# Kernel optimization log

Measured on AMD Instinct MI355X. Metric: run time of the kernel, lower is better.

## Reference

```python
import jax, jax.numpy as jnp
import numpy as np

WIDTH = 384
STEP_SIZE = 0.1  # hard-coded in EnergyBlock.__init__
EPS = 1e-5


def conv1d(x, w):
    # x: [B, Cin, L], w: [Cout, Cin, K], stride 1, SAME padding (padding=1 for k=3)
    return jax.lax.conv_general_dilated(
        x, w, window_strides=(1,), padding='SAME',
        dimension_numbers=('NCH', 'OIH', 'NCH'))


def layer_norm_cl(x):
    # torch layer_norm over shape[1:] == normalize jointly over (C, L) per batch elem,
    # no affine params, biased variance.
    mu = jnp.mean(x, axis=(1, 2), keepdims=True)
    var = jnp.mean(jnp.square(x - mu), axis=(1, 2), keepdims=True)
    return (x - mu) * jax.lax.rsqrt(var + EPS)


def energy_block(cat, op_w):
    # cat: [B, width+1, L] = concat(interim_thought, x)
    xl = layer_norm_cl(cat[:, :WIDTH])          # post-LN x (the grad variable)
    c = conv1d(cat, op_w)                        # operator(inputs): no path through xl
    # Ex = sum(c * xl) + sum(where(xl>=0, xl^2, 0))
    # dEx/dxl = c + 2*relu(xl)  (analytic; matches torch.autograd.grad)
    grads = c + 2.0 * jnp.maximum(xl, 0.0)
    return xl - STEP_SIZE * grads


def _init_conv(key, cout, cin, k=3):
    scale = (1.0 / (cin * k)) ** 0.5
    return jax.random.uniform(key, (cout, cin, k), jnp.float32, -scale, scale)


def setup_inputs() -> dict:
    key = jax.random.key(0)
    ks = jax.random.split(key, 6)
    B, L = 32, 512
    return {
        'x': jax.random.normal(ks[0], (B, 1, L), jnp.float32),
        'iters_to_do': 16,
        'proj_w': _init_conv(ks[1], WIDTH, 1),
        'op_w': _init_conv(ks[2], WIDTH, WIDTH + 1),
        'h1_w': _init_conv(ks[3], WIDTH, WIDTH),
        'h2_w': _init_conv(ks[4], WIDTH // 2, WIDTH),
        'h3_w': _init_conv(ks[5], 2, WIDTH // 2),
    }


def reference(x, iters_to_do, proj_w, op_w, h1_w, h2_w, h3_w):
    relu = jax.nn.relu
    interim = relu(conv1d(x, proj_w))  # initial_thought [B, width, L]

    def step(it, _):
        cat = jnp.concatenate([it, x], axis=1)       # recall=True
        new_it = energy_block(cat, op_w)
        out = conv1d(relu(conv1d(relu(conv1d(new_it, h1_w)), h2_w)), h3_w)  # [B,2,L]
        return new_it, out

    _, outs = jax.lax.scan(step, interim, None, length=iters_to_do)
    # eval mode: return all_outputs [B, iters, 2, L]
    return jnp.transpose(outs, (1, 0, 2, 3))
```

## Files before the change

kernel.cpp:

```cpp
#include <hip/hip_runtime.h>
#include <hip/hip_bf16.h>

#define BB 32
#define WW 384
#define LL 512
#define ITERS 16
#define NPB (WW * LL)
#define LROWS 514
#define RP (LROWS * 8)

typedef __attribute__((ext_vector_type(8))) short bf16x8;
typedef __attribute__((ext_vector_type(4))) float f32x4;

__device__ __forceinline__ float b2f(short s) {
    unsigned u = ((unsigned)(unsigned short)s) << 16;
    float f;
    __builtin_memcpy(&f, &u, 4);
    return f;
}
__device__ __forceinline__ short f2b(float v) {
    __hip_bfloat16 h = __float2bfloat16(v);
    return *(short*)&h;
}

__device__ __forceinline__ void gld16(const short* g, short* l) {
    __builtin_amdgcn_global_load_lds(
        (const __attribute__((address_space(1))) unsigned int*)g,
        (__attribute__((address_space(3))) unsigned int*)l, 16, 0, 0);
}

__global__ void wsplit_op(const float* __restrict__ w, short* __restrict__ wh) {
    int i = blockIdx.x * 256 + threadIdx.x;
    if (i >= 3 * 48 * 384 * 8) return;
    int e = i & 7, co = (i >> 3) % 384, oct = (i >> 3) / 384 % 48,
        tap = i / (8 * 384 * 48);
    int ci = oct * 8 + e;
    wh[i] = f2b(w[(co * 385 + ci) * 3 + tap]);
}

__global__ void wx_prep(const float* __restrict__ w, float* __restrict__ wx) {
    int i = blockIdx.x * 256 + threadIdx.x;
    if (i >= 3 * 384) return;
    int co = i % 384, tap = i / 384;
    wx[tap * 384 + co] = w[(co * 385 + 384) * 3 + tap];
}

__global__ void wsplit_h(const float* __restrict__ w, short* __restrict__ wh,
                         int COD, int CO_real) {
    int i = blockIdx.x * 256 + threadIdx.x;
    if (i >= 3 * 48 * COD * 8) return;
    int e = i & 7, co = (i >> 3) % COD, oct = (i >> 3) / COD % 48,
        tap = i / (8 * COD * 48);
    int ci = oct * 8 + e;
    float v = (co < CO_real) ? w[(co * 384 + ci) * 3 + tap] : 0.f;
    wh[i] = f2b(v);
}

__global__ void init_rows(short* itAh, short* itAl, short* itBh, short* itBl,
                          short* a1A, short* a1B, short* a2A, short* a2B) {
    int row = (blockIdx.x & 1) ? (LROWS - 1) : 0;
    int b = blockIdx.x >> 1;
    int tid = threadIdx.x;
    for (int i = tid; i < 48 * 8; i += 64) {
        size_t o = (size_t)b * 48 * RP + (size_t)(i >> 3) * RP + row * 8 + (i & 7);
        itAh[o] = 0; itAl[o] = 0; itBh[o] = 0; itBl[o] = 0;
        a1A[o] = 0; a1B[o] = 0;
    }
    for (int i = tid; i < 24 * 8; i += 64) {
        size_t o = (size_t)b * 24 * RP + (size_t)(i >> 3) * RP + row * 8 + (i & 7);
        a2A[o] = 0; a2B[o] = 0;
    }
}

__global__ void zero_part(float* part, int n) {
    int i = blockIdx.x * 256 + threadIdx.x;
    if (i < n) part[i] = 0.f;
}

__global__ __launch_bounds__(256) void proj_relu(const float* __restrict__ x,
                                                 const float* __restrict__ wp,
                                                 short* __restrict__ oh,
                                                 short* __restrict__ ol,
                                                 float* __restrict__ part) {
    int b = blockIdx.x >> 3, sl = blockIdx.x & 7;
    int tid = threadIdx.x;
    __shared__ float ws[WW * 3];
    __shared__ float xs[66];
    for (int i = tid; i < WW * 3; i += 256) ws[i] = wp[i];
    int l0 = sl * 64;
    for (int i = tid; i < 66; i += 256) {
        int l = l0 + i - 1;
        xs[i] = (l >= 0 && l < LL) ? x[b * LL + l] : 0.f;
    }
    __syncthreads();
    size_t sb = (size_t)b * 48 * RP;
    float s = 0.f, sq = 0.f;
    for (int idx = tid; idx < 64 * WW; idx += 256) {
        int lo = idx / WW, co = idx % WW;
        float v = fmaxf(ws[co * 3] * xs[lo] + ws[co * 3 + 1] * xs[lo + 1] +
                            ws[co * 3 + 2] * xs[lo + 2], 0.f);
        size_t o = sb + (size_t)(co >> 3) * RP + (l0 + lo + 1) * 8 + (co & 7);
        __hip_bfloat16 h = __float2bfloat16(v);
        oh[o] = *(short*)&h;
        ol[o] = f2b(v - __bfloat162float(h));
        s += v; sq += v * v;
    }
    #pragma unroll
    for (int off = 32; off > 0; off >>= 1) {
        s += __shfl_down(s, off);
        sq += __shfl_down(sq, off);
    }
    __shared__ float sr[8];
    int w = tid >> 6;
    if ((tid & 63) == 0) { sr[w] = s; sr[4 + w] = sq; }
    __syncthreads();
    if (tid == 0) {
        atomicAdd(&part[b * 2], sr[0] + sr[1] + sr[2] + sr[3]);
        atomicAdd(&part[b * 2 + 1], sr[4] + sr[5] + sr[6] + sr[7]);
    }
}


#define MMAC(A, B, MT, NT)                                                 \
    acc[MT][NT] = __builtin_amdgcn_mfma_f32_16x16x32_bf16(A, B,            \
                                                          acc[MT][NT], 0, 0, 0);

#define STAGE(KC, TB)                                                      \
    do {                                                                   \
        short* sb_ = smem + (TB) * ASZ;                                    \
        _Pragma("unroll")                                                  \
        for (int r_ = 0; r_ < (ANS + 3) / 4; r_++) {                       \
            int s_ = r_ * 4 + wn;                                          \
            if (s_ < ANS) {                                                \
                int u0_ = s_ * 64;                                         \
                if (u0_ > AU - 64) u0_ = AU - 64;                          \
                int u_ = u0_ + lane;                                       \
                int oc_ = u_ / TLROWS;                                     \
                int rw_ = u_ - oc_ * TLROWS;                               \
                gld16(inh + ibase + (size_t)((KC) * 4 + oc_) * RP +        \
                          (size_t)(l0 + rw_) * 8,                          \
                      sb_ + u0_ * 8);                                      \
            }                                                              \
        }                                                                  \
    } while (0)

#define DECL_B(S) bf16x8 fb0##S, fb1##S, fb2##S, fb3##S;

#define LOADB(S, T, KC)                                                    \
    do {                                                                   \
        const short* bp_ = wh + ((((size_t)(T) * CHUNKS + (KC)) * 4 + q) * \
                                     COD + co0w + lane15) * 8;             \
        fb0##S = *(const bf16x8*)(bp_);                                    \
        fb1##S = *(const bf16x8*)(bp_ + 16 * 8);                           \
        fb2##S = *(const bf16x8*)(bp_ + 32 * 8);                           \
        fb3##S = *(const bf16x8*)(bp_ + 48 * 8);                           \
    } while (0)

#define COMP_TAP(SB, T, S)                                                 \
    do {                                                                   \
        const short* As_ = (SB);                                           \
        int ar_ = q * TLROWS + wl + lane15 + (T);                          \
        bf16x8 fa0 = *(const bf16x8*)(As_ + ar_ * 8);                      \
        bf16x8 fa1 = *(const bf16x8*)(As_ + (ar_ + 16) * 8);               \
        bf16x8 fa2 = *(const bf16x8*)(As_ + (ar_ + 32) * 8);               \
        bf16x8 fa3 = *(const bf16x8*)(As_ + (ar_ + 48) * 8);               \
        MMAC(fa0, fb0##S, 0, 0) MMAC(fa0, fb1##S, 0, 1)                    \
        MMAC(fa0, fb2##S, 0, 2) MMAC(fa0, fb3##S, 0, 3)                    \
        MMAC(fa1, fb0##S, 1, 0) MMAC(fa1, fb1##S, 1, 1)                    \
        MMAC(fa1, fb2##S, 1, 2) MMAC(fa1, fb3##S, 1, 3)                    \
        MMAC(fa2, fb0##S, 2, 0) MMAC(fa2, fb1##S, 2, 1)                    \
        MMAC(fa2, fb2##S, 2, 2) MMAC(fa2, fb3##S, 2, 3)                    \
        MMAC(fa3, fb0##S, 3, 0) MMAC(fa3, fb1##S, 3, 1)                    \
        MMAC(fa3, fb2##S, 3, 2) MMAC(fa3, fb3##S, 3, 3)                    \
    } while (0)

template <int CHUNKS, int IOCT, int OOCT, int COD, int MODE, int LSPLIT>
__device__ __forceinline__ void conv_body(
    int bid, short* smem,
    const short* __restrict__ inh, const short* __restrict__ inl,
    const short* __restrict__ wh, const float* __restrict__ xf,
    const float* __restrict__ wx, const float* __restrict__ part_in,
    float* __restrict__ part_out, short* __restrict__ outh,
    short* __restrict__ outl) {
    constexpr int TLROWS = LSPLIT ? 258 : 130;
    constexpr int ASZ = 4 * TLROWS * 8;
    constexpr int AU = 4 * TLROWS;
    constexpr int ANS = (AU + 63) / 64;

    int tid = threadIdx.x;
    int lane = tid & 63;
    int wn = __builtin_amdgcn_readfirstlane(tid >> 6);
    int lane15 = lane & 15, q = lane >> 4;
    int b, l0, co0, wl, wco;
    if (LSPLIT) {
        int ct = bid >> 6, g = bid & 63;
        b = g >> 1; l0 = (g & 1) * 256; co0 = ct * 64;
        wl = wn * 64; wco = 0;
    } else {
        int ct = bid >> 7, g = bid & 127;
        b = g >> 2; l0 = (g & 3) * 128; co0 = ct * 128;
        wl = (wn >> 1) * 64; wco = (wn & 1) * 64;
    }
    const int co0w = co0 + wco;
    const size_t ibase = (size_t)b * IOCT * RP;

    f32x4 acc[4][4];
    #pragma unroll
    for (int i = 0; i < 4; i++)
        #pragma unroll
        for (int j = 0; j < 4; j++) acc[i][j] = (f32x4){0.f, 0.f, 0.f, 0.f};

    DECL_B(X)
    DECL_B(Y)
    DECL_B(Z)
    STAGE(0, 0);
    LOADB(X, 0, 0);
    LOADB(Y, 1, 0);
    __syncthreads();
    #pragma unroll 2
    for (int kc = 0; kc < CHUNKS; kc++) {
        int cur = kc & 1;
        if (kc + 1 < CHUNKS) STAGE(kc + 1, cur ^ 1);
        LOADB(Z, 2, kc);
        short* sb = smem + cur * ASZ;
        COMP_TAP(sb, 0, X);
        if (kc + 1 < CHUNKS) LOADB(X, 0, kc + 1);
        COMP_TAP(sb, 1, Y);
        if (kc + 1 < CHUNKS) LOADB(Y, 1, kc + 1);
        COMP_TAP(sb, 2, Z);
        __syncthreads();
    }

    int l0w = l0 + wl;
    const size_t obase = (size_t)b * OOCT * RP;
    if constexpr (MODE == 1) {
        float s_in = part_in[b * 2], sq_in = part_in[b * 2 + 1];
        float mu = s_in / (float)NPB;
        float var = sq_in / (float)NPB - mu * mu;
        float rs = rsqrtf(var + 1e-5f);
        const float* xb = xf + b * LL;
        float s = 0.f, sq = 0.f;
        #pragma unroll
        for (int nt = 0; nt < 4; nt++) {
            int n = co0w + nt * 16 + lane15;
            float w0 = wx[n], w1 = wx[384 + n], w2 = wx[768 + n];
            #pragma unroll
            for (int mt = 0; mt < 4; mt++)
                #pragma unroll
                for (int r = 0; r < 4; r++) {
                    int m = mt * 16 + q * 4 + r;
                    int l = l0w + m;
                    size_t idx = ibase + (size_t)(n >> 3) * RP +
                                 (l + 1) * 8 + (n & 7);
                    float xm1 = (l > 0) ? xb[l - 1] : 0.f;
                    float xp1 = (l < LL - 1) ? xb[l + 1] : 0.f;
                    float c = acc[mt][nt][r] + w0 * xm1 + w1 * xb[l] + w2 * xp1;
                    float itv = b2f(inh[idx]) + b2f(inl[idx]);
                    float xl = (itv - mu) * rs;
                    float nv = xl - 0.1f * c - 0.2f * fmaxf(xl, 0.f);
                    s += nv;
                    sq += nv * nv;
                    __hip_bfloat16 h = __float2bfloat16(nv);
                    outh[idx] = *(short*)&h;
                    outl[idx] = f2b(nv - __bfloat162float(h));
                }
        }
        #pragma unroll
        for (int off = 32; off > 0; off >>= 1) {
            s += __shfl_down(s, off);
            sq += __shfl_down(sq, off);
        }
        __shared__ float sr[8];
        if (lane == 0) { sr[wn] = s; sr[4 + wn] = sq; }
        __syncthreads();
        if (tid == 0) {
            atomicAdd(&part_out[b * 2], sr[0] + sr[1] + sr[2] + sr[3]);
            atomicAdd(&part_out[b * 2 + 1], sr[4] + sr[5] + sr[6] + sr[7]);
        }
    } else {
        #pragma unroll
        for (int mt = 0; mt < 4; mt++)
            #pragma unroll
            for (int nt = 0; nt < 4; nt++)
                #pragma unroll
                for (int r = 0; r < 4; r++) {
                    int m = mt * 16 + q * 4 + r;
                    int n = co0w + nt * 16 + lane15;
                    size_t idx = obase + (size_t)(n >> 3) * RP +
                                 (l0w + m + 1) * 8 + (n & 7);
                    outh[idx] = f2b(fmaxf(acc[mt][nt][r], 0.f));
                }
    }
}

__global__ __launch_bounds__(128) void h3k(const short* __restrict__ a2,
                                           const float* __restrict__ w3,
                                           float* __restrict__ out, int t) {
    __shared__ float ws3[2 * 192 * 3];
    int tid = threadIdx.x;
    for (int i = tid; i < 2 * 192 * 3; i += 128) ws3[i] = w3[i];
    __syncthreads();
    int b = blockIdx.x >> 3, sl = blockIdx.x & 7;
    int l = sl * 64 + (tid >> 1);
    int ch = tid & 1;
    const short* ab = a2 + (size_t)b * 24 * RP;
    const float* wc = ws3 + ch * 576;
    float a = 0.f;
    #pragma unroll 4
    for (int oct = 0; oct < 24; oct++) {
        const short* p = ab + (size_t)oct * RP + l * 8;
        bf16x8 v0 = *(const bf16x8*)p;
        bf16x8 v1 = *(const bf16x8*)(p + 8);
        bf16x8 v2 = *(const bf16x8*)(p + 16);
        #pragma unroll
        for (int j = 0; j < 8; j++) {
            const float* wp = wc + (oct * 8 + j) * 3;
            a += wp[0] * b2f(v0[j]) + wp[1] * b2f(v1[j]) + wp[2] * b2f(v2[j]);
        }
    }
    out[(((size_t)b * ITERS + t) * 2 + ch) * LL + l] = a;
}

__global__ __launch_bounds__(256, 3) void fusedF(
    const short* __restrict__ ch, const short* __restrict__ cl,
    short* __restrict__ nh, short* __restrict__ nl,
    const short* __restrict__ wOph, const short* __restrict__ wH1,
    const short* __restrict__ wH2, const float* __restrict__ xf,
    const float* __restrict__ wx, const float* __restrict__ part_in,
    float* __restrict__ part_out, short* __restrict__ a1w,
    const short* __restrict__ a1r, short* __restrict__ a2w,
    int opB, int h1B) {
    __shared__ __align__(16) short smem[2 * 4 * 258 * 8];
    int bid = blockIdx.x;
    if (bid < opB) {
        conv_body<12, 48, 48, 384, 1, 0>(bid, smem, ch, cl, wOph, xf, wx,
                                         part_in, part_out, nh, nl);
    } else if (bid < opB + h1B) {
        conv_body<12, 48, 48, 384, 0, 0>(bid - opB, smem, ch, nullptr, wH1,
                                         nullptr, nullptr, nullptr, nullptr,
                                         a1w, nullptr);
    } else {
        conv_body<12, 48, 24, 192, 0, 1>(bid - opB - h1B, smem, a1r, nullptr,
                                         wH2, nullptr, nullptr, nullptr,
                                         nullptr, a2w, nullptr);
    }
}

extern "C" void kernel_launch(void* const* d_in, const int* in_sizes, int n_in,
                              void* d_out, int out_size, void* d_ws, size_t ws_size,
                              hipStream_t stream) {
    const float* x = (const float*)d_in[0];
    const float* proj_w = (const float*)d_in[2];
    const float* op_w = (const float*)d_in[3];
    const float* h1_w = (const float*)d_in[4];
    const float* h2_w = (const float*)d_in[5];
    const float* h3_w = (const float*)d_in[6];
    float* out = (float*)d_out;

    char* base = (char*)d_ws;
    size_t off = 0;
    auto alloc = [&](size_t bytes) {
        char* p = base + off;
        off += (bytes + 255) & ~(size_t)255;
        return p;
    };
    const size_t ITB = (size_t)BB * 48 * RP * 2;
    short* itAh = (short*)alloc(ITB);
    short* itAl = (short*)alloc(ITB);
    short* itBh = (short*)alloc(ITB);
    short* itBl = (short*)alloc(ITB);
    short* a1A = (short*)alloc((size_t)BB * 48 * RP * 2);
    short* a1B = (short*)alloc((size_t)BB * 48 * RP * 2);
    short* a2A = (short*)alloc((size_t)BB * 24 * RP * 2);
    short* a2B = (short*)alloc((size_t)BB * 24 * RP * 2);
    short* wOph = (short*)alloc((size_t)3 * 48 * 384 * 8 * 2);
    short* wH1 = (short*)alloc((size_t)3 * 48 * 384 * 8 * 2);
    short* wH2 = (short*)alloc((size_t)3 * 48 * 192 * 8 * 2);
    float* wx = (float*)alloc((size_t)3 * 384 * 4);
    float* part = (float*)alloc((size_t)(ITERS + 1) * 64 * 4);
    if (off > ws_size) return;

    wsplit_op<<<(3 * 48 * 384 * 8 + 255) / 256, 256, 0, stream>>>(op_w, wOph);
    wx_prep<<<5, 256, 0, stream>>>(op_w, wx);
    wsplit_h<<<(3 * 48 * 384 * 8 + 255) / 256, 256, 0, stream>>>(h1_w, wH1, 384, 384);
    wsplit_h<<<(3 * 48 * 192 * 8 + 255) / 256, 256, 0, stream>>>(h2_w, wH2, 192, 192);
    init_rows<<<BB * 2, 64, 0, stream>>>(itAh, itAl, itBh, itBl, a1A, a1B,
                                         a2A, a2B);
    zero_part<<<5, 256, 0, stream>>>(part, (ITERS + 1) * 64);
    proj_relu<<<BB * 8, 256, 0, stream>>>(x, proj_w, itAh, itAl, part);

    short* a1buf[2] = {a1A, a1B};
    short* a2buf[2] = {a2A, a2B};
    short *ch = itAh, *cl = itAl, *nh = itBh, *nl = itBl;
    for (int t = 0; t < ITERS + 2; t++) {
        int opB = (t < ITERS) ? 384 : 0;
        int h1B = (t >= 1 && t <= ITERS) ? 384 : 0;
        int h2B = (t >= 2 && t <= ITERS + 1) ? 192 : 0;
        int tp = (t < ITERS) ? t : 0;
        fusedF<<<opB + h1B + h2B, 256, 0, stream>>>(
            ch, cl, nh, nl, wOph, wH1, wH2, x, wx, part + tp * 64,
            part + (tp + 1) * 64, a1buf[(t - 1) & 1], a1buf[(t - 2) & 1],
            a2buf[(t - 2) & 1], opB, h1B);
        if (t >= 3)
            h3k<<<256, 128, 0, stream>>>(a2buf[(t - 3) & 1], h3_w, out, t - 3);
        if (t < ITERS) {
            short* th = ch; ch = nh; nh = th;
            short* tl = cl; cl = nl; nl = tl;
        }
    }
    h3k<<<256, 128, 0, stream>>>(a2buf[(ITERS - 1) & 1], h3_w, out, ITERS - 1);
}
```

Measured before the change: 1.073 ms.

## Give each wave private double-buffered LDS staging and drop block barriers

Each wave now stages only the 66 input rows it needs into its own private double-buffered LDS region, so the per-chunk __syncthreads is removed from the conv main loop. Weight-fragment loads are rescheduled around sched_barriers, and the MFMA bursts are wrapped in s_setprio to favour matrix issue. This is meant to cut barrier stalls and LDS footprint, which could allow more blocks per CU. In exchange, waves that share L rows now load duplicate input data, and correctness depends on the hardware or compiler waiting for the async global-to-LDS loads without an explicit barrier.

```diff
diff --git a/kernel.cpp b/kernel.cpp
--- a/kernel.cpp
+++ b/kernel.cpp
@@ -127,20 +127,16 @@
 
 #define STAGE(KC, TB)                                                      \
     do {                                                                   \
-        short* sb_ = smem + (TB) * ASZ;                                    \
+        short* sb_ = wsmem + (TB) * ASZW;                                  \
         _Pragma("unroll")                                                  \
-        for (int r_ = 0; r_ < (ANS + 3) / 4; r_++) {                       \
-            int s_ = r_ * 4 + wn;                                          \
-            if (s_ < ANS) {                                                \
-                int u0_ = s_ * 64;                                         \
-                if (u0_ > AU - 64) u0_ = AU - 64;                          \
-                int u_ = u0_ + lane;                                       \
-                int oc_ = u_ / TLROWS;                                     \
-                int rw_ = u_ - oc_ * TLROWS;                               \
-                gld16(inh + ibase + (size_t)((KC) * 4 + oc_) * RP +        \
-                          (size_t)(l0 + rw_) * 8,                          \
-                      sb_ + u0_ * 8);                                      \
-            }                                                              \
+        for (int s_ = 0; s_ < 5; s_++) {                                   \
+            int u0_ = (s_ < 4) ? s_ * 64 : 200;                            \
+            int u_ = u0_ + lane;                                           \
+            int oc_ = u_ / 66;                                             \
+            int rw_ = u_ - oc_ * 66;                                       \
+            gld16(inh + ibase + (size_t)((KC) * 4 + oc_) * RP +            \
+                      (size_t)(l0w + rw_) * 8,                             \
+                  sb_ + u0_ * 8);                                          \
         }                                                                  \
     } while (0)
 
@@ -159,11 +155,12 @@
 #define COMP_TAP(SB, T, S)                                                 \
     do {                                                                   \
         const short* As_ = (SB);                                           \
-        int ar_ = q * TLROWS + wl + lane15 + (T);                          \
+        int ar_ = q * 66 + lane15 + (T);                                   \
         bf16x8 fa0 = *(const bf16x8*)(As_ + ar_ * 8);                      \
         bf16x8 fa1 = *(const bf16x8*)(As_ + (ar_ + 16) * 8);               \
         bf16x8 fa2 = *(const bf16x8*)(As_ + (ar_ + 32) * 8);               \
         bf16x8 fa3 = *(const bf16x8*)(As_ + (ar_ + 48) * 8);               \
+        __builtin_amdgcn_s_setprio(1);                                     \
         MMAC(fa0, fb0##S, 0, 0) MMAC(fa0, fb1##S, 0, 1)                    \
         MMAC(fa0, fb2##S, 0, 2) MMAC(fa0, fb3##S, 0, 3)                    \
         MMAC(fa1, fb0##S, 1, 0) MMAC(fa1, fb1##S, 1, 1)                    \
@@ -172,6 +169,7 @@
         MMAC(fa2, fb2##S, 2, 2) MMAC(fa2, fb3##S, 2, 3)                    \
         MMAC(fa3, fb0##S, 3, 0) MMAC(fa3, fb1##S, 3, 1)                    \
         MMAC(fa3, fb2##S, 3, 2) MMAC(fa3, fb3##S, 3, 3)                    \
+        __builtin_amdgcn_s_setprio(0);                                     \
     } while (0)
 
 template <int CHUNKS, int IOCT, int OOCT, int COD, int MODE, int LSPLIT>
@@ -182,10 +180,7 @@
     const float* __restrict__ wx, const float* __restrict__ part_in,
     float* __restrict__ part_out, short* __restrict__ outh,
     short* __restrict__ outl) {
-    constexpr int TLROWS = LSPLIT ? 258 : 130;
-    constexpr int ASZ = 4 * TLROWS * 8;
-    constexpr int AU = 4 * TLROWS;
-    constexpr int ANS = (AU + 63) / 64;
+    constexpr int ASZW = 4 * 66 * 8;
 
     int tid = threadIdx.x;
     int lane = tid & 63;
@@ -202,7 +197,9 @@
         wl = (wn >> 1) * 64; wco = (wn & 1) * 64;
     }
     const int co0w = co0 + wco;
+    const int l0w = l0 + wl;
     const size_t ibase = (size_t)b * IOCT * RP;
+    short* wsmem = smem + wn * (2 * ASZW);
 
     f32x4 acc[4][4];
     #pragma unroll
@@ -215,23 +212,24 @@
     DECL_B(Z)
     STAGE(0, 0);
     LOADB(X, 0, 0);
-    LOADB(Y, 1, 0);
-    __syncthreads();
-    #pragma unroll 2
+    asm volatile("s_waitcnt vmcnt(0)" ::: "memory");
+    __builtin_amdgcn_sched_barrier(0);
+    #pragma unroll 1
     for (int kc = 0; kc < CHUNKS; kc++) {
-        int cur = kc & 1;
-        if (kc + 1 < CHUNKS) STAGE(kc + 1, cur ^ 1);
+        short* sb = wsmem + (kc & 1) * ASZW;
+        if (kc + 1 < CHUNKS) STAGE(kc + 1, (kc & 1) ^ 1);
+        LOADB(Y, 1, kc);
+        __builtin_amdgcn_sched_barrier(0);
+        COMP_TAP(sb, 0, X);
         LOADB(Z, 2, kc);
-        short* sb = smem + cur * ASZ;
-        COMP_TAP(sb, 0, X);
+        __builtin_amdgcn_sched_barrier(0);
+        COMP_TAP(sb, 1, Y);
         if (kc + 1 < CHUNKS) LOADB(X, 0, kc + 1);
-        COMP_TAP(sb, 1, Y);
-        if (kc + 1 < CHUNKS) LOADB(Y, 1, kc + 1);
+        __builtin_amdgcn_sched_barrier(0);
         COMP_TAP(sb, 2, Z);
-        __syncthreads();
-    }
-
-    int l0w = l0 + wl;
+        __builtin_amdgcn_sched_barrier(0);
+    }
+
     const size_t obase = (size_t)b * OOCT * RP;
     if constexpr (MODE == 1) {
         float s_in = part_in[b * 2], sq_in = part_in[b * 2 + 1];
@@ -330,7 +328,7 @@
     float* __restrict__ part_out, short* __restrict__ a1w,
     const short* __restrict__ a1r, short* __restrict__ a2w,
     int opB, int h1B) {
-    __shared__ __align__(16) short smem[2 * 4 * 258 * 8];
+    __shared__ __align__(16) short smem[4 * 2 * 4 * 66 * 8];
     int bid = blockIdx.x;
     if (bid < opB) {
         conv_body<12, 48, 48, 384, 1, 0>(bid, smem, ch, cl, wOph, xf, wx,
```

New measurement: 1.276 ms. 18.9% more time.
